# Performance work log

Measured on AMD Instinct MI355X. Metric: run time of the kernel, lower is better.

## Reference

```python
import jax, jax.numpy as jnp
import numpy as np

N_REL = 32
N_ATTR = 8
WIDTH = 256
N_ENT = 2048


def setup_inputs() -> dict:
    key = jax.random.key(0)
    k1, k2, k3 = jax.random.split(key, 3)
    database = jax.random.uniform(k1, (N_REL, N_ENT, N_ENT), dtype=jnp.float32)
    attributes = jax.random.uniform(k2, (N_ATTR, N_ENT), dtype=jnp.float32)
    weights = jax.random.normal(k3, (2 * N_REL + N_ATTR, WIDTH), dtype=jnp.float32)
    return {"database": database, "attributes": attributes, "weights": weights}


def reference(database, attributes, weights):
    # per-relation reductions over each entity dim: [R, N] each
    q = jnp.concatenate([
        database.sum(axis=1),          # sum over dim 1 -> [R, N]
        database.sum(axis=2),          # sum over dim 2 -> [R, N]
        attributes * 2.0,              # [A, N]
    ], axis=0)                          # [2R + A, N]
    quantified = 1.0 - jnp.exp(-q)
    # softmax over rows of weights (axis 0), then [W, 2R+A] @ [2R+A, N]
    w = jax.nn.softmax(weights, axis=0)
    outputs = jnp.einsum('kw,kn->wn', w, quantified)  # [WIDTH, N]
    return outputs, quantified
```

## Files before the change

kernel.cpp:

```cpp
#include <hip/hip_runtime.h>
#include <math.h>

#define NREL  32
#define NENT  2048
#define NATTR 8
#define WIDTH 256
#define NK    (2 * NREL + NATTR)
#define CHUNKS_OUT 16
#define SUBS  4

typedef float f4 __attribute__((ext_vector_type(4)));

__global__ __launch_bounds__(256) void reduce_db_kernel(
    const float* __restrict__ db,
    float* __restrict__ qout,
    float* __restrict__ partial,
    int rowsPerWave,
    int nSubs)
{
    const int bx   = blockIdx.x;
    const int r    = bx >> 4;
    const int cOut = bx & (CHUNKS_OUT - 1);
    const int tid  = threadIdx.x;
    const int wave = tid >> 6;
    const int lane = tid & 63;

    __shared__ __align__(16) float smem[4][NENT];
    float (*rpart)[33] = reinterpret_cast<float(*)[33]>(&smem[0][0]);

    const size_t rowStride = NENT / 4;
    const f4* relBase = reinterpret_cast<const f4*>(db)
                      + (size_t)r * NENT * rowStride
                      + (size_t)(cOut * 128) * rowStride
                      + lane;

    f4 acc[8];
#pragma unroll
    for (int k = 0; k < 8; ++k) acc[k] = (f4)0.f;

    for (int sc = 0; sc < nSubs; ++sc) {
        const int i0 = sc * 32;
        const f4* base = relBase
                       + (size_t)(i0 + wave * rowsPerWave) * rowStride;

        for (int j = 0; j < rowsPerWave; j += 2) {
            const f4* rowA = base + (size_t)j * rowStride;
            const f4* rowB = rowA + rowStride;
            float rsA = 0.f, rsB = 0.f;
#pragma unroll
            for (int k = 0; k < 8; ++k) {
                f4 v = __builtin_nontemporal_load(rowA + k * 64);
                acc[k] += v;
                rsA += (v.x + v.y) + (v.z + v.w);
            }
#pragma unroll
            for (int k = 0; k < 8; ++k) {
                f4 v = __builtin_nontemporal_load(rowB + k * 64);
                acc[k] += v;
                rsB += (v.x + v.y) + (v.z + v.w);
            }
            rpart[lane][wave * rowsPerWave + j]     = rsA;
            rpart[lane][wave * rowsPerWave + j + 1] = rsB;
        }
        __syncthreads();

        {
            const int row = tid >> 3;
            const int seg = tid & 7;
            float t = 0.f;
#pragma unroll
            for (int i = 0; i < 8; ++i) t += rpart[seg * 8 + i][row];
            t += __shfl_xor(t, 1, 64);
            t += __shfl_xor(t, 2, 64);
            t += __shfl_xor(t, 4, 64);
            if (seg == 0)
                qout[(size_t)(NREL + r) * NENT + cOut * 128 + i0 + row] =
                    1.f - __expf(-t);
        }
        __syncthreads();
    }

#pragma unroll
    for (int k = 0; k < 8; ++k)
        *reinterpret_cast<f4*>(&smem[wave][k * 256 + lane * 4]) = acc[k];
    __syncthreads();

    f4* part4 = reinterpret_cast<f4*>(partial) + (size_t)bx * rowStride;
    for (int g = tid; g < NENT / 4; g += 256) {
        f4 a0 = *reinterpret_cast<const f4*>(&smem[0][g * 4]);
        f4 a1 = *reinterpret_cast<const f4*>(&smem[1][g * 4]);
        f4 a2 = *reinterpret_cast<const f4*>(&smem[2][g * 4]);
        f4 a3 = *reinterpret_cast<const f4*>(&smem[3][g * 4]);
        part4[g] = (a0 + a1) + (a2 + a3);
    }
}

#define MM_BLOCKS  ((WIDTH / 32) * (NENT / 128))
#define FIN_BLOCKS ((NREL + NATTR) * NENT / 256)

__global__ __launch_bounds__(256) void tail_kernel(
    const float* __restrict__ partial,
    const float* __restrict__ attrs,
    const float* __restrict__ W,
    float* __restrict__ qout,
    float* __restrict__ out)
{
    const int b   = blockIdx.x;
    const int tid = threadIdx.x;

    if (b < MM_BLOCKS) {
        __shared__ __align__(16) float qt[NK][132];
        __shared__ float wsl[NK][33];
        const int wg = b >> 4;
        const int cg = b & 15;
        const int w0 = wg * 32;
        const int c0 = cg * 128;
        const int cq = c0 >> 2;

        const f4* part4  = reinterpret_cast<const f4*>(partial);
        const f4* qout4  = reinterpret_cast<const f4*>(qout);
        const f4* attrs4 = reinterpret_cast<const f4*>(attrs);

        for (int i = tid; i < NK * 32; i += 256) {
            const int k  = i >> 5;
            const int cf = i & 31;
            f4 q;
            if (k < NREL) {
                f4 sum = (f4)0.f;
#pragma unroll
                for (int c = 0; c < CHUNKS_OUT; ++c)
                    sum += part4[(size_t)(k * CHUNKS_OUT + c) * 512 + cq + cf];
                q.x = 1.f - __expf(-sum.x); q.y = 1.f - __expf(-sum.y);
                q.z = 1.f - __expf(-sum.z); q.w = 1.f - __expf(-sum.w);
            } else if (k < 2 * NREL) {
                q = qout4[(size_t)k * 512 + cq + cf];
            } else {
                f4 v = attrs4[(size_t)(k - 2 * NREL) * 512 + cq + cf];
                q.x = 1.f - __expf(-2.f * v.x); q.y = 1.f - __expf(-2.f * v.y);
                q.z = 1.f - __expf(-2.f * v.z); q.w = 1.f - __expf(-2.f * v.w);
            }
            *reinterpret_cast<f4*>(&qt[k][cf * 4]) = q;
        }
        for (int i = tid; i < NK * 32; i += 256) {
            const int k  = i >> 5;
            const int wl = i & 31;
            wsl[k][wl] = W[k * WIDTH + w0 + wl];
        }
        __syncthreads();

        if (tid < 32) {
            const int wl = tid;
            float m = wsl[0][wl];
#pragma unroll
            for (int k = 1; k < NK; ++k) m = fmaxf(m, wsl[k][wl]);
            float s = 0.f;
            float e[NK];
#pragma unroll
            for (int k = 0; k < NK; ++k) { e[k] = __expf(wsl[k][wl] - m); s += e[k]; }
            const float inv = 1.f / s;
#pragma unroll
            for (int k = 0; k < NK; ++k) wsl[k][wl] = e[k] * inv;
        }
        __syncthreads();

        const int wl = tid >> 3;
        const int cl = (tid & 7) * 16;
        f4 a0 = (f4)0.f, a1 = (f4)0.f, a2 = (f4)0.f, a3 = (f4)0.f;
#pragma unroll 8
        for (int k = 0; k < NK; ++k) {
            const float s = wsl[k][wl];
            const f4* row = reinterpret_cast<const f4*>(&qt[k][cl]);
            f4 v0 = row[0], v1 = row[1], v2 = row[2], v3 = row[3];
            a0 += s * v0; a1 += s * v1; a2 += s * v2; a3 += s * v3;
        }
        f4* o4 = reinterpret_cast<f4*>(out + (size_t)(w0 + wl) * NENT + c0 + cl);
        o4[0] = a0; o4[1] = a1; o4[2] = a2; o4[3] = a3;
    } else {
        const int idx = (b - MM_BLOCKS) * 256 + tid;
        const int row = idx >> 11;
        const int n   = idx & (NENT - 1);
        if (row < NREL) {
            float s = 0.f;
#pragma unroll
            for (int c = 0; c < CHUNKS_OUT; ++c)
                s += partial[((size_t)(row * CHUNKS_OUT + c) << 11) + n];
            qout[((size_t)row << 11) + n] = 1.f - __expf(-s);
        } else {
            const int a = row - NREL;
            float v = attrs[((size_t)a << 11) + n];
            qout[((size_t)(2 * NREL + a) << 11) + n] = 1.f - __expf(-2.f * v);
        }
    }
}

extern "C" void kernel_launch(void* const* d_in, const int* in_sizes, int n_in,
                              void* d_out, int out_size, void* d_ws, size_t ws_size,
                              hipStream_t stream)
{
    const float* db    = (const float*)d_in[0];
    const float* attrs = (const float*)d_in[1];
    const float* W     = (const float*)d_in[2];

    float* out   = (float*)d_out;
    float* quant = out + (size_t)WIDTH * NENT;

    float* partial = (float*)d_ws;

    reduce_db_kernel<<<NREL * CHUNKS_OUT, 256, 0, stream>>>(
        db, quant, partial, 8, SUBS);
    tail_kernel<<<MM_BLOCKS + FIN_BLOCKS, 256, 0, stream>>>(
        partial, attrs, W, quant, out);
}
```

Baseline: 100.6 us.

## Merge sub-chunk loop into one pass and fold finalize blocks into matmul tail

The reduce kernel now handles all 128 rows per block in a single pass: each wave covers 32 rows, the row-sum partials go to a larger 64x129 shared buffer, and only one barrier-and-reduce phase runs instead of four. The column-sum and attribute finalize blocks are removed from the tail kernel; the blocks with wg==0 write the quantified rows while building their tiles. This removes repeated barriers and extra blocks, at the cost of more shared memory per block (about 65 KB), which may lower occupancy in the bandwidth-bound reduction.

```diff
diff --git a/kernel.cpp b/kernel.cpp
--- a/kernel.cpp
+++ b/kernel.cpp
@@ -7,7 +7,6 @@
 #define WIDTH 256
 #define NK    (2 * NREL + NATTR)
 #define CHUNKS_OUT 16
-#define SUBS  4
 
 typedef float f4 __attribute__((ext_vector_type(4)));
 
@@ -15,8 +14,7 @@
     const float* __restrict__ db,
     float* __restrict__ qout,
     float* __restrict__ partial,
-    int rowsPerWave,
-    int nSubs)
+    int rowsPerWave)
 {
     const int bx   = blockIdx.x;
     const int r    = bx >> 4;
@@ -25,78 +23,68 @@
     const int wave = tid >> 6;
     const int lane = tid & 63;
 
-    __shared__ __align__(16) float smem[4][NENT];
-    float (*rpart)[33] = reinterpret_cast<float(*)[33]>(&smem[0][0]);
+    __shared__ float rpart[64][129];
+    __shared__ __align__(16) float csmem[4][NENT];
 
     const size_t rowStride = NENT / 4;
-    const f4* relBase = reinterpret_cast<const f4*>(db)
-                      + (size_t)r * NENT * rowStride
-                      + (size_t)(cOut * 128) * rowStride
-                      + lane;
+    const f4* base = reinterpret_cast<const f4*>(db)
+                   + (size_t)r * NENT * rowStride
+                   + (size_t)(cOut * 128 + wave * rowsPerWave) * rowStride
+                   + lane;
 
     f4 acc[8];
 #pragma unroll
     for (int k = 0; k < 8; ++k) acc[k] = (f4)0.f;
 
-    for (int sc = 0; sc < nSubs; ++sc) {
-        const int i0 = sc * 32;
-        const f4* base = relBase
-                       + (size_t)(i0 + wave * rowsPerWave) * rowStride;
+    for (int jj = 0; jj < rowsPerWave; jj += 2) {
+        const f4* rowA = base + (size_t)jj * rowStride;
+        const f4* rowB = rowA + rowStride;
+        float rsA = 0.f, rsB = 0.f;
+#pragma unroll
+        for (int k = 0; k < 8; ++k) {
+            f4 v = __builtin_nontemporal_load(rowA + k * 64);
+            acc[k] += v;
+            rsA += (v.x + v.y) + (v.z + v.w);
+        }
+#pragma unroll
+        for (int k = 0; k < 8; ++k) {
+            f4 v = __builtin_nontemporal_load(rowB + k * 64);
+            acc[k] += v;
+            rsB += (v.x + v.y) + (v.z + v.w);
+        }
+        rpart[lane][wave * rowsPerWave + jj]     = rsA;
+        rpart[lane][wave * rowsPerWave + jj + 1] = rsB;
+    }
+    __syncthreads();
 
-        for (int j = 0; j < rowsPerWave; j += 2) {
-            const f4* rowA = base + (size_t)j * rowStride;
-            const f4* rowB = rowA + rowStride;
-            float rsA = 0.f, rsB = 0.f;
+    {
+        const int row  = tid >> 1;
+        const int half = tid & 1;
+        float s = 0.f;
 #pragma unroll
-            for (int k = 0; k < 8; ++k) {
-                f4 v = __builtin_nontemporal_load(rowA + k * 64);
-                acc[k] += v;
-                rsA += (v.x + v.y) + (v.z + v.w);
-            }
-#pragma unroll
-            for (int k = 0; k < 8; ++k) {
-                f4 v = __builtin_nontemporal_load(rowB + k * 64);
-                acc[k] += v;
-                rsB += (v.x + v.y) + (v.z + v.w);
-            }
-            rpart[lane][wave * rowsPerWave + j]     = rsA;
-            rpart[lane][wave * rowsPerWave + j + 1] = rsB;
-        }
-        __syncthreads();
-
-        {
-            const int row = tid >> 3;
-            const int seg = tid & 7;
-            float t = 0.f;
-#pragma unroll
-            for (int i = 0; i < 8; ++i) t += rpart[seg * 8 + i][row];
-            t += __shfl_xor(t, 1, 64);
-            t += __shfl_xor(t, 2, 64);
-            t += __shfl_xor(t, 4, 64);
-            if (seg == 0)
-                qout[(size_t)(NREL + r) * NENT + cOut * 128 + i0 + row] =
-                    1.f - __expf(-t);
-        }
-        __syncthreads();
+        for (int i = 0; i < 32; ++i) s += rpart[half * 32 + i][row];
+        s += __shfl_xor(s, 1, 64);
+        if (half == 0)
+            qout[(size_t)(NREL + r) * NENT + cOut * 128 + row] =
+                1.f - __expf(-s);
     }
 
 #pragma unroll
     for (int k = 0; k < 8; ++k)
-        *reinterpret_cast<f4*>(&smem[wave][k * 256 + lane * 4]) = acc[k];
+        *reinterpret_cast<f4*>(&csmem[wave][k * 256 + lane * 4]) = acc[k];
     __syncthreads();
 
     f4* part4 = reinterpret_cast<f4*>(partial) + (size_t)bx * rowStride;
     for (int g = tid; g < NENT / 4; g += 256) {
-        f4 a0 = *reinterpret_cast<const f4*>(&smem[0][g * 4]);
-        f4 a1 = *reinterpret_cast<const f4*>(&smem[1][g * 4]);
-        f4 a2 = *reinterpret_cast<const f4*>(&smem[2][g * 4]);
-        f4 a3 = *reinterpret_cast<const f4*>(&smem[3][g * 4]);
+        f4 a0 = *reinterpret_cast<const f4*>(&csmem[0][g * 4]);
+        f4 a1 = *reinterpret_cast<const f4*>(&csmem[1][g * 4]);
+        f4 a2 = *reinterpret_cast<const f4*>(&csmem[2][g * 4]);
+        f4 a3 = *reinterpret_cast<const f4*>(&csmem[3][g * 4]);
         part4[g] = (a0 + a1) + (a2 + a3);
     }
 }
 
 #define MM_BLOCKS  ((WIDTH / 32) * (NENT / 128))
-#define FIN_BLOCKS ((NREL + NATTR) * NENT / 256)
 
 __global__ __launch_bounds__(256) void tail_kernel(
     const float* __restrict__ partial,
@@ -108,89 +96,75 @@
     const int b   = blockIdx.x;
     const int tid = threadIdx.x;
 
-    if (b < MM_BLOCKS) {
-        __shared__ __align__(16) float qt[NK][132];
-        __shared__ float wsl[NK][33];
-        const int wg = b >> 4;
-        const int cg = b & 15;
-        const int w0 = wg * 32;
-        const int c0 = cg * 128;
-        const int cq = c0 >> 2;
+    __shared__ __align__(16) float qt[NK][132];
+    __shared__ float wsl[NK][33];
+    const int wg = b >> 4;
+    const int cg = b & 15;
+    const int w0 = wg * 32;
+    const int c0 = cg * 128;
+    const int cq = c0 >> 2;
 
-        const f4* part4  = reinterpret_cast<const f4*>(partial);
-        const f4* qout4  = reinterpret_cast<const f4*>(qout);
-        const f4* attrs4 = reinterpret_cast<const f4*>(attrs);
+    const f4* part4  = reinterpret_cast<const f4*>(partial);
+    const f4* qout4  = reinterpret_cast<const f4*>(qout);
+    const f4* attrs4 = reinterpret_cast<const f4*>(attrs);
+    f4*       qoutw4 = reinterpret_cast<f4*>(qout);
 
-        for (int i = tid; i < NK * 32; i += 256) {
-            const int k  = i >> 5;
-            const int cf = i & 31;
-            f4 q;
-            if (k < NREL) {
-                f4 sum = (f4)0.f;
-#pragma unroll
-                for (int c = 0; c < CHUNKS_OUT; ++c)
-                    sum += part4[(size_t)(k * CHUNKS_OUT + c) * 512 + cq + cf];
-                q.x = 1.f - __expf(-sum.x); q.y = 1.f - __expf(-sum.y);
-                q.z = 1.f - __expf(-sum.z); q.w = 1.f - __expf(-sum.w);
-            } else if (k < 2 * NREL) {
-                q = qout4[(size_t)k * 512 + cq + cf];
-            } else {
-                f4 v = attrs4[(size_t)(k - 2 * NREL) * 512 + cq + cf];
-                q.x = 1.f - __expf(-2.f * v.x); q.y = 1.f - __expf(-2.f * v.y);
-                q.z = 1.f - __expf(-2.f * v.z); q.w = 1.f - __expf(-2.f * v.w);
-            }
-            *reinterpret_cast<f4*>(&qt[k][cf * 4]) = q;
-        }
-        for (int i = tid; i < NK * 32; i += 256) {
-            const int k  = i >> 5;
-            const int wl = i & 31;
-            wsl[k][wl] = W[k * WIDTH + w0 + wl];
-        }
-        __syncthreads();
-
-        if (tid < 32) {
-            const int wl = tid;
-            float m = wsl[0][wl];
-#pragma unroll
-            for (int k = 1; k < NK; ++k) m = fmaxf(m, wsl[k][wl]);
-            float s = 0.f;
-            float e[NK];
-#pragma unroll
-            for (int k = 0; k < NK; ++k) { e[k] = __expf(wsl[k][wl] - m); s += e[k]; }
-            const float inv = 1.f / s;
-#pragma unroll
-            for (int k = 0; k < NK; ++k) wsl[k][wl] = e[k] * inv;
-        }
-        __syncthreads();
-
-        const int wl = tid >> 3;
-        const int cl = (tid & 7) * 16;
-        f4 a0 = (f4)0.f, a1 = (f4)0.f, a2 = (f4)0.f, a3 = (f4)0.f;
-#pragma unroll 8
-        for (int k = 0; k < NK; ++k) {
-            const float s = wsl[k][wl];
-            const f4* row = reinterpret_cast<const f4*>(&qt[k][cl]);
-            f4 v0 = row[0], v1 = row[1], v2 = row[2], v3 = row[3];
-            a0 += s * v0; a1 += s * v1; a2 += s * v2; a3 += s * v3;
-        }
-        f4* o4 = reinterpret_cast<f4*>(out + (size_t)(w0 + wl) * NENT + c0 + cl);
-        o4[0] = a0; o4[1] = a1; o4[2] = a2; o4[3] = a3;
-    } else {
-        const int idx = (b - MM_BLOCKS) * 256 + tid;
-        const int row = idx >> 11;
-        const int n   = idx & (NENT - 1);
-        if (row < NREL) {
-            float s = 0.f;
+    for (int i = tid; i < NK * 32; i += 256) {
+        const int k  = i >> 5;
+        const int cf = i & 31;
+        f4 q;
+        if (k < NREL) {
+            f4 sum = (f4)0.f;
 #pragma unroll
             for (int c = 0; c < CHUNKS_OUT; ++c)
-                s += partial[((size_t)(row * CHUNKS_OUT + c) << 11) + n];
-            qout[((size_t)row << 11) + n] = 1.f - __expf(-s);
+                sum += part4[(size_t)(k * CHUNKS_OUT + c) * 512 + cq + cf];
+            q.x = 1.f - __expf(-sum.x); q.y = 1.f - __expf(-sum.y);
+            q.z = 1.f - __expf(-sum.z); q.w = 1.f - __expf(-sum.w);
+            if (wg == 0) qoutw4[(size_t)k * 512 + cq + cf] = q;
+        } else if (k < 2 * NREL) {
+            q = qout4[(size_t)k * 512 + cq + cf];
         } else {
-            const int a = row - NREL;
-            float v = attrs[((size_t)a << 11) + n];
-            qout[((size_t)(2 * NREL + a) << 11) + n] = 1.f - __expf(-2.f * v);
+            f4 v = attrs4[(size_t)(k - 2 * NREL) * 512 + cq + cf];
+            q.x = 1.f - __expf(-2.f * v.x); q.y = 1.f - __expf(-2.f * v.y);
+            q.z = 1.f - __expf(-2.f * v.z); q.w = 1.f - __expf(-2.f * v.w);
+            if (wg == 0) qoutw4[(size_t)k * 512 + cq + cf] = q;
         }
+        *reinterpret_cast<f4*>(&qt[k][cf * 4]) = q;
     }
+    for (int i = tid; i < NK * 32; i += 256) {
+        const int k  = i >> 5;
+        const int wl = i & 31;
+        wsl[k][wl] = W[k * WIDTH + w0 + wl];
+    }
+    __syncthreads();
+
+    if (tid < 32) {
+        const int wl = tid;
+        float m = wsl[0][wl];
+#pragma unroll
+        for (int k = 1; k < NK; ++k) m = fmaxf(m, wsl[k][wl]);
+        float s = 0.f;
+        float e[NK];
+#pragma unroll
+        for (int k = 0; k < NK; ++k) { e[k] = __expf(wsl[k][wl] - m); s += e[k]; }
+        const float inv = 1.f / s;
+#pragma unroll
+        for (int k = 0; k < NK; ++k) wsl[k][wl] = e[k] * inv;
+    }
+    __syncthreads();
+
+    const int wl = tid >> 3;
+    const int cl = (tid & 7) * 16;
+    f4 a0 = (f4)0.f, a1 = (f4)0.f, a2 = (f4)0.f, a3 = (f4)0.f;
+#pragma unroll 8
+    for (int k = 0; k < NK; ++k) {
+        const float s = wsl[k][wl];
+        const f4* row = reinterpret_cast<const f4*>(&qt[k][cl]);
+        f4 v0 = row[0], v1 = row[1], v2 = row[2], v3 = row[3];
+        a0 += s * v0; a1 += s * v1; a2 += s * v2; a3 += s * v3;
+    }
+    f4* o4 = reinterpret_cast<f4*>(out + (size_t)(w0 + wl) * NENT + c0 + cl);
+    o4[0] = a0; o4[1] = a1; o4[2] = a2; o4[3] = a3;
 }
 
 extern "C" void kernel_launch(void* const* d_in, const int* in_sizes, int n_in,
@@ -207,7 +181,7 @@
     float* partial = (float*)d_ws;
 
     reduce_db_kernel<<<NREL * CHUNKS_OUT, 256, 0, stream>>>(
-        db, quant, partial, 8, SUBS);
-    tail_kernel<<<MM_BLOCKS + FIN_BLOCKS, 256, 0, stream>>>(
+        db, quant, partial, 32);
+    tail_kernel<<<MM_BLOCKS, 256, 0, stream>>>(
         partial, attrs, W, quant, out);
 }
```

New measurement: 99.85 us. Within noise of the previous version (-0.8%).
